# Performance work log

Measured on AMD Instinct MI355X. Metric: run time of the kernel, lower is better.

The kernel has to match this reference:

```python
import jax, jax.numpy as jnp
import numpy as np

D = 768
H0, H1 = 1536, 768  # mlp_layers '1536,768'


def setup_inputs() -> dict:
    key = jax.random.key(0)
    ks = jax.random.split(key, 8)
    bsz, C, l_x, l_y = 8, 64, 256, 256
    xs = jax.random.normal(ks[0], (bsz, l_x, D), dtype=jnp.float32)
    ys = jax.random.normal(ks[1], (bsz, C, l_y, D), dtype=jnp.float32)
    # torch.nn.Linear weights: [out_features, in_features]
    def lin(k, fout, fin):
        bound = 1.0 / np.sqrt(fin)
        kw, kb = jax.random.split(k)
        W = jax.random.uniform(kw, (fout, fin), jnp.float32, -bound, bound)
        b = jax.random.uniform(kb, (fout,), jnp.float32, -bound, bound)
        return W, b
    W0, b0 = lin(ks[2], H0, 2 * D)
    W1, b1 = lin(ks[3], H1, H0)
    W2, b2 = lin(ks[4], 1, H1)
    return {"xs": xs, "ys": ys, "W0": W0, "b0": b0, "W1": W1, "b1": b1, "W2": W2, "b2": b2}


def reference(xs, ys, W0, b0, W1, b1, W2, b2):
    bsz, l_x, d = xs.shape
    _, C, l_y, _ = ys.shape
    # dot-product scores: [bsz, C, l_x, l_y]
    scores = jnp.einsum('bxd,bcyd->bcxy', xs, ys)
    argmax_idx = jnp.argmax(scores, axis=-1)  # [bsz, C, l_x]
    # gather winning y vector for each x token: [bsz, C, l_x, d]
    idx = jnp.broadcast_to(argmax_idx[..., None], (bsz, C, l_x, d))
    y_sel = jnp.take_along_axis(ys, idx, axis=2)
    xs_exp = jnp.broadcast_to(xs[:, None], (bsz, C, l_x, d))
    # stack then flatten(start_dim=-2) == concat along last dim: [bsz,C,l_x,2d]
    h = jnp.concatenate([xs_exp, y_sel], axis=-1)
    # MLP (dropout is identity at inference)
    h = jax.nn.softplus(jnp.einsum('bcxi,oi->bcxo', h, W0) + b0)
    h = jax.nn.softplus(jnp.einsum('bcxi,oi->bcxo', h, W1) + b1)
    s = jnp.einsum('bcxi,oi->bcxo', h, W2) + b2  # [bsz,C,l_x,1]
    return jnp.sum(s[..., 0], axis=-1)  # [bsz, C]
```

## Files before the change

kernel.cpp:

```cpp
#include <hip/hip_runtime.h>
#include <stdint.h>

#define DB   8
#define DC   64
#define DLX  256
#define DLY  256
#define DD   768
#define DH0  1536
#define DH1  768
#define NBC  (DB*DC)
#define NTOK (NBC*DLX)
#define TAU  0.25f

typedef float f32x4 __attribute__((ext_vector_type(4)));
typedef _Float16 f16x8 __attribute__((ext_vector_type(8)));
typedef _Float16 f16x4 __attribute__((ext_vector_type(4)));

__device__ __forceinline__ float softplusf(float x){
  float t = __builtin_amdgcn_exp2f(-fabsf(x) * 1.44269504f);
  return fmaxf(x, 0.0f) + 0.69314718f * __builtin_amdgcn_logf(1.0f + t);
}

__device__ __forceinline__ void gload_lds16(const void* g, void* l){
  __builtin_amdgcn_global_load_lds((const __attribute__((address_space(1))) void*)g,
                                   (__attribute__((address_space(3))) void*)l,
                                   16, 0, 0);
}

__global__ __launch_bounds__(256) void k_cvt16(const float* __restrict__ src, int ld, int off,
                                               int rows, int cols, _Float16* __restrict__ dst){
  int total = rows * (cols >> 3);
  for (int idx = blockIdx.x * 256 + threadIdx.x; idx < total; idx += gridDim.x * 256){
    int r = idx / (cols >> 3), c8 = (idx % (cols >> 3)) * 8;
    const float* s = src + (size_t)r * ld + off + c8;
    float4 f0 = *(const float4*)s, f1 = *(const float4*)(s + 4);
    f16x8 v;
    v[0]=(_Float16)f0.x; v[1]=(_Float16)f0.y; v[2]=(_Float16)f0.z; v[3]=(_Float16)f0.w;
    v[4]=(_Float16)f1.x; v[5]=(_Float16)f1.y; v[6]=(_Float16)f1.z; v[7]=(_Float16)f1.w;
    *(f16x8*)(dst + (size_t)r * cols + c8) = v;
  }
}

__global__ __launch_bounds__(1024, 1) void k_scores3(const _Float16* __restrict__ xs16,
                                                     const _Float16* __restrict__ ys16,
                                                     const float* __restrict__ xs,
                                                     const float* __restrict__ ys,
                                                     int* __restrict__ widx){
  const int bc = blockIdx.y, b = bc >> 6;
  const int x0 = blockIdx.x * 128;
  const float* X = xs + ((size_t)b * DLX + x0) * DD;
  const float* Y = ys + (size_t)bc * DLY * DD;
  __shared__ __align__(16) _Float16 As[128 * 32];
  __shared__ __align__(16) _Float16 Bs[256 * 32];
  __shared__ float rmx[128][4];
  __shared__ float gm[128];
  __shared__ unsigned short cand[128][8];
  __shared__ int ccnt[128];
  const int tid = threadIdx.x;
  const int l = tid & 63, w = tid >> 6;
  const int wr = w >> 2, wc = w & 3;
  const int lrow = l & 15, lg = l >> 4;
  const int kq = (lg ^ (lrow & 3)) * 8;
  const int srow = l >> 2;
  const int kg = (((l & 3) ^ ((l >> 2) & 3))) * 8;
  const _Float16* srcB = ys16 + ((size_t)bc * DLY + w*16 + srow) * DD + kg;
  const _Float16* srcA = xs16 + ((size_t)b * DLX + x0 + (w & 7)*16 + srow) * DD + kg;

  f32x4 acc[2][4];
  #pragma unroll
  for (int i = 0; i < 2; i++)
    #pragma unroll
    for (int j = 0; j < 4; j++) acc[i][j] = (f32x4){0.f,0.f,0.f,0.f};

  for (int k0 = 0; k0 < DD; k0 += 32){
    __syncthreads();
    gload_lds16(srcB + k0, Bs + w*512);
    if (w < 8) gload_lds16(srcA + k0, As + w*512);
    __syncthreads();
    f16x8 af[2], bf[4];
    #pragma unroll
    for (int i = 0; i < 2; i++)
      af[i] = *(const f16x8*)&As[(wr*32 + i*16 + lrow)*32 + kq];
    #pragma unroll
    for (int j = 0; j < 4; j++)
      bf[j] = *(const f16x8*)&Bs[(wc*64 + j*16 + lrow)*32 + kq];
    #pragma unroll
    for (int i = 0; i < 2; i++)
      #pragma unroll
      for (int j = 0; j < 4; j++)
        acc[i][j] = __builtin_amdgcn_mfma_f32_16x16x32_f16(af[i], bf[j], acc[i][j], 0, 0, 0);
  }

  #pragma unroll
  for (int i = 0; i < 2; i++)
    #pragma unroll
    for (int r = 0; r < 4; r++){
      float m = fmaxf(fmaxf(acc[i][0][r], acc[i][1][r]), fmaxf(acc[i][2][r], acc[i][3][r]));
      m = fmaxf(m, __shfl_xor(m, 1));
      m = fmaxf(m, __shfl_xor(m, 2));
      m = fmaxf(m, __shfl_xor(m, 4));
      m = fmaxf(m, __shfl_xor(m, 8));
      if (lrow == 0) rmx[wr*32 + i*16 + lg*4 + r][wc] = m;
    }
  __syncthreads();
  if (tid < 128){
    gm[tid] = fmaxf(fmaxf(rmx[tid][0], rmx[tid][1]), fmaxf(rmx[tid][2], rmx[tid][3]));
    ccnt[tid] = 0;
  }
  __syncthreads();
  #pragma unroll
  for (int i = 0; i < 2; i++)
    #pragma unroll
    for (int r = 0; r < 4; r++){
      int t = wr*32 + i*16 + lg*4 + r;
      float thr = gm[t] - TAU;
      #pragma unroll
      for (int j = 0; j < 4; j++){
        float s = acc[i][j][r];
        if (s >= thr){
          int p = atomicAdd(&ccnt[t], 1);
          if (p < 8) cand[t][p] = (unsigned short)(wc*64 + j*16 + lrow);
        }
      }
    }
  __syncthreads();
  for (int it = 0; it < 8; it++){
    int t = w * 8 + it;
    int cnt = ccnt[t];
    int by;
    if (cnt == 1){
      by = cand[t][0];
    } else {
      const float* xr = X + (size_t)t * DD;
      float best = -1e30f; int besty = 0;
      int n = (cnt <= 8) ? cnt : 256;
      for (int p = 0; p < n; p++){
        int c = (cnt <= 8) ? (int)cand[t][p] : p;
        const float* yr = Y + (size_t)c * DD;
        float s = 0.f;
        #pragma unroll
        for (int q = 0; q < 3; q++){
          float4 xv = *(const float4*)(xr + l*12 + q*4);
          float4 yv = *(const float4*)(yr + l*12 + q*4);
          s += xv.x*yv.x + xv.y*yv.y + xv.z*yv.z + xv.w*yv.w;
        }
        s += __shfl_xor(s, 1);  s += __shfl_xor(s, 2);  s += __shfl_xor(s, 4);
        s += __shfl_xor(s, 8);  s += __shfl_xor(s, 16); s += __shfl_xor(s, 32);
        if (s > best || (s == best && c < besty)){ best = s; besty = c; }
      }
      by = besty;
    }
    if (l == 0) widx[(size_t)bc * DLX + x0 + t] = by;
  }
}

template<int MODE>
__global__ __launch_bounds__(512) void k_gemm16(const _Float16* __restrict__ A,
        unsigned bdelta,
        const int* __restrict__ widx,
        const _Float16* __restrict__ X0h,
        const float* __restrict__ bias,
        const float* __restrict__ w2,
        float* __restrict__ outF,
        _Float16* __restrict__ outH){
  constexpr int K = (MODE == 2) ? DH0 : DD;
  __shared__ __align__(16) _Float16 As[128 * 64];
  __shared__ __align__(16) _Float16 Bs[256 * 64];
  const int tid = threadIdx.x;
  const int gx = gridDim.x, nwg = gx * gridDim.y;
  int lin = blockIdx.x + gx * blockIdx.y;
  int swz = (lin & 7) * (nwg >> 3) + (lin >> 3);
  const int n0  = (swz % gx) * 256;
  const int by  = swz / gx;
  const int rt0 = by * 128;
  const int l = tid & 63, w = tid >> 6;
  const int wr = w >> 2, wc = w & 3;
  const int lrow = l & 15, lg = l >> 4;

  int bc = 0, xb = 0, b = 0;
  if constexpr (MODE == 1){ bc = by >> 1; xb = (by & 1) * 128; b = bc >> 6; }

  const int urow = l >> 3;
  const int uslot = (l & 7) ^ (urow & 7);
  unsigned goff[6];
  _Float16* ldst[6];
  #pragma unroll
  for (int i = 0; i < 6; i++){
    int u = w*6 + i;
    if (u < 16){
      int row = u*8 + urow;
      unsigned aoff;
      if constexpr (MODE == 1){
        int yi = widx[bc * DLX + xb + row];
        aoff = (unsigned)((bc * DLY + yi) * DD);
      } else {
        aoff = (unsigned)((rt0 + row) * K);
      }
      goff[i] = aoff + uslot*8;
      ldst[i] = (_Float16*)As + u*512;
    } else {
      int row = (u - 16)*8 + urow;
      goff[i] = bdelta + (unsigned)((n0 + row) * K) + uslot*8;
      ldst[i] = (_Float16*)Bs + (u - 16)*512;
    }
  }

  f32x4 acc[4][4];
  #pragma unroll
  for (int i = 0; i < 4; i++)
    #pragma unroll
    for (int j = 0; j < 4; j++) acc[i][j] = (f32x4){0.f,0.f,0.f,0.f};

  for (int k0 = 0; k0 < K; k0 += 64){
    __syncthreads();
    #pragma unroll
    for (int i = 0; i < 6; i++)
      gload_lds16(A + (size_t)(goff[i] + (unsigned)k0), ldst[i]);
    __syncthreads();
    #pragma unroll
    for (int kh = 0; kh < 2; kh++){
      const int rc = ((kh*4 + lg) ^ (lrow & 7)) * 8;
      f16x8 af[4], bf[4];
      #pragma unroll
      for (int i = 0; i < 4; i++){
        af[i] = *(const f16x8*)&As[(wr*64 + i*16 + lrow)*64 + rc];
        bf[i] = *(const f16x8*)&Bs[(wc*64 + i*16 + lrow)*64 + rc];
      }
      #pragma unroll
      for (int i = 0; i < 4; i++)
        #pragma unroll
        for (int j = 0; j < 4; j++)
          acc[i][j] = __builtin_amdgcn_mfma_f32_16x16x32_f16(af[i], bf[j], acc[i][j], 0, 0, 0);
    }
  }

  if constexpr (MODE == 0){
    #pragma unroll
    for (int mi = 0; mi < 4; mi++)
      #pragma unroll
      for (int ni = 0; ni < 4; ni++){
        int n = n0 + wc*64 + ni*16 + lrow;
        float bv = bias[n];
        #pragma unroll
        for (int r = 0; r < 4; r++){
          int m = wr*64 + mi*16 + lg*4 + r;
          outH[(size_t)(rt0 + m) * DH0 + n] = (_Float16)(acc[mi][ni][r] + bv);
        }
      }
  } else if constexpr (MODE == 1){
    #pragma unroll
    for (int mi = 0; mi < 4; mi++)
      #pragma unroll
      for (int ni = 0; ni < 4; ni++){
        int n = n0 + wc*64 + ni*16 + lrow;
        #pragma unroll
        for (int r = 0; r < 4; r++){
          int m = wr*64 + mi*16 + lg*4 + r;
          float x0v = (float)X0h[((size_t)b * DLX + xb + m) * DH0 + n];
          float v = softplusf(acc[mi][ni][r] + x0v);
          outH[(size_t)(rt0 + m) * DH0 + n] = (_Float16)v;
        }
      }
  } else {
    float p[4][4];
    #pragma unroll
    for (int mi = 0; mi < 4; mi++)
      #pragma unroll
      for (int r = 0; r < 4; r++) p[mi][r] = 0.f;
    #pragma unroll
    for (int ni = 0; ni < 4; ni++){
      int n = n0 + wc*64 + ni*16 + lrow;
      float b1v = bias[n], w2v = w2[n];
      #pragma unroll
      for (int mi = 0; mi < 4; mi++)
        #pragma unroll
        for (int r = 0; r < 4; r++)
          p[mi][r] += softplusf(acc[mi][ni][r] + b1v) * w2v;
    }
    const int nb = (int)(swz % gx);
    #pragma unroll
    for (int mi = 0; mi < 4; mi++)
      #pragma unroll
      for (int r = 0; r < 4; r++){
        float s = p[mi][r];
        s += __shfl_xor(s, 1);
        s += __shfl_xor(s, 2);
        s += __shfl_xor(s, 4);
        s += __shfl_xor(s, 8);
        if (lrow == 0){
          size_t t = (size_t)rt0 + wr*64 + mi*16 + lg*4 + r;
          outF[t * 12 + nb*4 + wc] = s;
        }
      }
  }
}

__global__ __launch_bounds__(256) void k_reduce(const float* __restrict__ spart,
                                                const float* __restrict__ b2,
                                                float* __restrict__ out){
  int bc = blockIdx.x, tid = threadIdx.x;
  const float* p = spart + ((size_t)bc * DLX + tid) * 12;
  float s = 0.0f;
  #pragma unroll
  for (int j = 0; j < 12; j++) s += p[j];
  __shared__ float red[256];
  red[tid] = s;
  __syncthreads();
  for (int off = 128; off > 0; off >>= 1){
    if (tid < off) red[tid] += red[tid + off];
    __syncthreads();
  }
  if (tid == 0) out[bc] = red[0] + 256.0f * b2[0];
}

extern "C" void kernel_launch(void* const* d_in, const int* in_sizes, int n_in,
                              void* d_out, int out_size, void* d_ws, size_t ws_size,
                              hipStream_t stream){
  const float* xs = (const float*)d_in[0];
  const float* ys = (const float*)d_in[1];
  const float* W0 = (const float*)d_in[2];
  const float* b0 = (const float*)d_in[3];
  const float* W1 = (const float*)d_in[4];
  const float* b1 = (const float*)d_in[5];
  const float* W2 = (const float*)d_in[6];
  const float* b2 = (const float*)d_in[7];
  float* out = (float*)d_out;

  char* wsp = (char*)d_ws;
  size_t off = 0;
  auto alloc = [&](size_t bytes)->void*{
    void* p = wsp + off;
    off += (bytes + 255) & ~(size_t)255;
    return p;
  };
  int* widx        = (int*)alloc((size_t)NTOK * 4);
  _Float16* ys16   = (_Float16*)alloc((size_t)NBC * DLY * DD * 2);
  _Float16* W0yf   = (_Float16*)alloc((size_t)DH0 * DD * 2);
  _Float16* xs16   = (_Float16*)alloc((size_t)DB * DLX * DD * 2);
  _Float16* W0xf   = (_Float16*)alloc((size_t)DH0 * DD * 2);
  _Float16* X0h    = (_Float16*)alloc((size_t)DB * DLX * DH0 * 2);
  float* spart     = (float*)alloc((size_t)NTOK * 12 * 4);
  _Float16* H0     = (_Float16*)alloc((size_t)NTOK * DH0 * 2);
  _Float16* W1f    = (_Float16*)alloc((size_t)DH1 * DH0 * 2);

  unsigned d0 = (unsigned)(W0xf - xs16);
  unsigned d1 = (unsigned)(W0yf - ys16);
  unsigned d2 = (unsigned)(W1f - H0);

  k_cvt16<<<dim3(576),  256, 0, stream>>>(W0, DH0, 0,  DH0, DD, W0xf);
  k_cvt16<<<dim3(576),  256, 0, stream>>>(W0, DH0, DD, DH0, DD, W0yf);
  k_cvt16<<<dim3(576),  256, 0, stream>>>(W1, DH0, 0,  DH1, DH0, W1f);
  k_cvt16<<<dim3(768),  256, 0, stream>>>(xs, DD, 0, DB*DLX, DD, xs16);
  k_cvt16<<<dim3(4096), 256, 0, stream>>>(ys, DD, 0, NBC*DLY, DD, ys16);
  k_scores3<<<dim3(2, NBC), 1024, 0, stream>>>(xs16, ys16, xs, ys, widx);
  k_gemm16<0><<<dim3(6, 16),   512, 0, stream>>>(xs16, d0, nullptr, nullptr, b0, nullptr, nullptr, X0h);
  k_gemm16<1><<<dim3(6, 1024), 512, 0, stream>>>(ys16, d1, widx, X0h, nullptr, nullptr, nullptr, H0);
  k_gemm16<2><<<dim3(3, 1024), 512, 0, stream>>>(H0, d2, nullptr, nullptr, b1, W2, spart, nullptr);
  k_reduce<<<NBC, 256, 0, stream>>>(spart, b2, out);
}
```

Baseline: 990.6 us.

## Fuse ys fp16 conversion into scores kernel and cover all x rows per block

The standalone ys fp32-to-fp16 conversion kernel is removed. The scores kernel now loads ys in fp32, converts it in registers, writes it to LDS for the MFMA and also stores the fp16 copy to global memory for the later GEMM. Each block now handles all 256 x rows of one (b,c) pair instead of 128, so ys is read once rather than twice. This removes a full pass over ys and a kernel launch, at the cost of a 4x4 accumulator tile per wave (more registers), synchronous global loads in place of direct-to-LDS loads, and a grid cut to 512 blocks.

```diff
diff --git a/kernel.cpp b/kernel.cpp
--- a/kernel.cpp
+++ b/kernel.cpp
@@ -41,82 +41,87 @@
   }
 }
 
-__global__ __launch_bounds__(1024, 1) void k_scores3(const _Float16* __restrict__ xs16,
-                                                     const _Float16* __restrict__ ys16,
+__global__ __launch_bounds__(1024, 2) void k_scores4(const _Float16* __restrict__ xs16,
+                                                     const float* __restrict__ ys,
                                                      const float* __restrict__ xs,
-                                                     const float* __restrict__ ys,
+                                                     _Float16* __restrict__ ys16,
                                                      int* __restrict__ widx){
-  const int bc = blockIdx.y, b = bc >> 6;
-  const int x0 = blockIdx.x * 128;
-  const float* X = xs + ((size_t)b * DLX + x0) * DD;
+  const int bc = blockIdx.x, b = bc >> 6;
   const float* Y = ys + (size_t)bc * DLY * DD;
-  __shared__ __align__(16) _Float16 As[128 * 32];
+  __shared__ __align__(16) _Float16 As[256 * 32];
   __shared__ __align__(16) _Float16 Bs[256 * 32];
-  __shared__ float rmx[128][4];
-  __shared__ float gm[128];
-  __shared__ unsigned short cand[128][8];
-  __shared__ int ccnt[128];
+  __shared__ float rmx[256][4];
+  __shared__ float gm[256];
+  __shared__ unsigned short cand[256][8];
+  __shared__ int ccnt[256];
   const int tid = threadIdx.x;
   const int l = tid & 63, w = tid >> 6;
   const int wr = w >> 2, wc = w & 3;
   const int lrow = l & 15, lg = l >> 4;
   const int kq = (lg ^ (lrow & 3)) * 8;
-  const int srow = l >> 2;
   const int kg = (((l & 3) ^ ((l >> 2) & 3))) * 8;
-  const _Float16* srcB = ys16 + ((size_t)bc * DLY + w*16 + srow) * DD + kg;
-  const _Float16* srcA = xs16 + ((size_t)b * DLX + x0 + (w & 7)*16 + srow) * DD + kg;
-
-  f32x4 acc[2][4];
-  #pragma unroll
-  for (int i = 0; i < 2; i++)
+  const _Float16* srcA = xs16 + ((size_t)b * DLX + w*16 + (l >> 2)) * DD + kg;
+  const int r = tid >> 2, c8 = (tid & 3) * 8;
+  const float* srcB = Y + (size_t)r * DD + c8;
+  _Float16* ydst = ys16 + ((size_t)bc * DLY + r) * DD + c8;
+  const int bslot = (((tid & 3) ^ (r & 3))) * 8;
+
+  f32x4 acc[4][4];
+  #pragma unroll
+  for (int i = 0; i < 4; i++)
     #pragma unroll
     for (int j = 0; j < 4; j++) acc[i][j] = (f32x4){0.f,0.f,0.f,0.f};
 
   for (int k0 = 0; k0 < DD; k0 += 32){
-    __syncthreads();
-    gload_lds16(srcB + k0, Bs + w*512);
-    if (w < 8) gload_lds16(srcA + k0, As + w*512);
-    __syncthreads();
-    f16x8 af[2], bf[4];
-    #pragma unroll
-    for (int i = 0; i < 2; i++)
-      af[i] = *(const f16x8*)&As[(wr*32 + i*16 + lrow)*32 + kq];
-    #pragma unroll
-    for (int j = 0; j < 4; j++)
-      bf[j] = *(const f16x8*)&Bs[(wc*64 + j*16 + lrow)*32 + kq];
-    #pragma unroll
-    for (int i = 0; i < 2; i++)
+    float4 f0 = *(const float4*)(srcB + k0);
+    float4 f1 = *(const float4*)(srcB + k0 + 4);
+    f16x8 hv;
+    hv[0]=(_Float16)f0.x; hv[1]=(_Float16)f0.y; hv[2]=(_Float16)f0.z; hv[3]=(_Float16)f0.w;
+    hv[4]=(_Float16)f1.x; hv[5]=(_Float16)f1.y; hv[6]=(_Float16)f1.z; hv[7]=(_Float16)f1.w;
+    __syncthreads();
+    gload_lds16(srcA + k0, As + w*512);
+    *(f16x8*)&Bs[r*32 + bslot] = hv;
+    *(f16x8*)(ydst + k0) = hv;
+    __syncthreads();
+    f16x8 af[4], bf[4];
+    #pragma unroll
+    for (int i = 0; i < 4; i++){
+      af[i] = *(const f16x8*)&As[(wr*64 + i*16 + lrow)*32 + kq];
+      bf[i] = *(const f16x8*)&Bs[(wc*64 + i*16 + lrow)*32 + kq];
+    }
+    #pragma unroll
+    for (int i = 0; i < 4; i++)
       #pragma unroll
       for (int j = 0; j < 4; j++)
         acc[i][j] = __builtin_amdgcn_mfma_f32_16x16x32_f16(af[i], bf[j], acc[i][j], 0, 0, 0);
   }
 
   #pragma unroll
-  for (int i = 0; i < 2; i++)
-    #pragma unroll
-    for (int r = 0; r < 4; r++){
-      float m = fmaxf(fmaxf(acc[i][0][r], acc[i][1][r]), fmaxf(acc[i][2][r], acc[i][3][r]));
+  for (int i = 0; i < 4; i++)
+    #pragma unroll
+    for (int r2 = 0; r2 < 4; r2++){
+      float m = fmaxf(fmaxf(acc[i][0][r2], acc[i][1][r2]), fmaxf(acc[i][2][r2], acc[i][3][r2]));
       m = fmaxf(m, __shfl_xor(m, 1));
       m = fmaxf(m, __shfl_xor(m, 2));
       m = fmaxf(m, __shfl_xor(m, 4));
       m = fmaxf(m, __shfl_xor(m, 8));
-      if (lrow == 0) rmx[wr*32 + i*16 + lg*4 + r][wc] = m;
+      if (lrow == 0) rmx[wr*64 + i*16 + lg*4 + r2][wc] = m;
     }
   __syncthreads();
-  if (tid < 128){
+  if (tid < 256){
     gm[tid] = fmaxf(fmaxf(rmx[tid][0], rmx[tid][1]), fmaxf(rmx[tid][2], rmx[tid][3]));
     ccnt[tid] = 0;
   }
   __syncthreads();
   #pragma unroll
-  for (int i = 0; i < 2; i++)
-    #pragma unroll
-    for (int r = 0; r < 4; r++){
-      int t = wr*32 + i*16 + lg*4 + r;
+  for (int i = 0; i < 4; i++)
+    #pragma unroll
+    for (int r2 = 0; r2 < 4; r2++){
+      int t = wr*64 + i*16 + lg*4 + r2;
       float thr = gm[t] - TAU;
       #pragma unroll
       for (int j = 0; j < 4; j++){
-        float s = acc[i][j][r];
+        float s = acc[i][j][r2];
         if (s >= thr){
           int p = atomicAdd(&ccnt[t], 1);
           if (p < 8) cand[t][p] = (unsigned short)(wc*64 + j*16 + lrow);
@@ -124,14 +129,14 @@
       }
     }
   __syncthreads();
-  for (int it = 0; it < 8; it++){
-    int t = w * 8 + it;
+  for (int it = 0; it < 16; it++){
+    int t = w * 16 + it;
     int cnt = ccnt[t];
     int by;
     if (cnt == 1){
       by = cand[t][0];
     } else {
-      const float* xr = X + (size_t)t * DD;
+      const float* xr = xs + ((size_t)b * DLX + t) * DD;
       float best = -1e30f; int besty = 0;
       int n = (cnt <= 8) ? cnt : 256;
       for (int p = 0; p < n; p++){
@@ -150,7 +155,7 @@
       }
       by = besty;
     }
-    if (l == 0) widx[(size_t)bc * DLX + x0 + t] = by;
+    if (l == 0) widx[(size_t)bc * DLX + t] = by;
   }
 }
 
@@ -351,8 +356,7 @@
   k_cvt16<<<dim3(576),  256, 0, stream>>>(W0, DH0, DD, DH0, DD, W0yf);
   k_cvt16<<<dim3(576),  256, 0, stream>>>(W1, DH0, 0,  DH1, DH0, W1f);
   k_cvt16<<<dim3(768),  256, 0, stream>>>(xs, DD, 0, DB*DLX, DD, xs16);
-  k_cvt16<<<dim3(4096), 256, 0, stream>>>(ys, DD, 0, NBC*DLY, DD, ys16);
-  k_scores3<<<dim3(2, NBC), 1024, 0, stream>>>(xs16, ys16, xs, ys, widx);
+  k_scores4<<<dim3(NBC), 1024, 0, stream>>>(xs16, ys, xs, ys16, widx);
   k_gemm16<0><<<dim3(6, 16),   512, 0, stream>>>(xs16, d0, nullptr, nullptr, b0, nullptr, nullptr, X0h);
   k_gemm16<1><<<dim3(6, 1024), 512, 0, stream>>>(ys16, d1, widx, X0h, nullptr, nullptr, nullptr, H0);
   k_gemm16<2><<<dim3(3, 1024), 512, 0, stream>>>(H0, d2, nullptr, nullptr, b1, W2, spart, nullptr);
```

Result: faster. 921.4 us (-7.0%).
